# Performance work log

Measured on AMD Instinct MI355X. Metric: run time of the kernel, lower is better.

Reference implementation:

```python
import jax, jax.numpy as jnp
import numpy as np

B, C, T = 16, 768, 1024
STEPS, NNEG, OFFSET = 12, 10, 1
COPIES = NNEG + 1


def setup_inputs() -> dict:
    key = jax.random.key(0)
    k1, k2, k3, k4 = jax.random.split(key, 4)
    x = jax.random.normal(k1, (B, C, T), jnp.float32)
    y = jax.random.normal(k2, (B, C, T), jnp.float32)
    # ConvTranspose2d(in_dim, out_dim, (1, steps)) weight -> [C_in, C_out, steps]
    W = jax.random.normal(k3, (C, C, STEPS), jnp.float32) * 0.02
    b = jnp.zeros((C,), jnp.float32)
    # Negative-sample indices, replicating torch sample_negatives (sample_distance=None):
    # randint in [0, T-1), bump collisions with the positive timestep, add per-batch offset.
    neg = jax.random.randint(k4, (B, NNEG * T), 0, T - 1)
    tszs = jnp.repeat(jnp.arange(T), NNEG)  # [NNEG*T]
    neg = jnp.where(neg >= tszs[None, :], neg + 1, neg)
    neg = neg + jnp.arange(B)[:, None] * T  # index into flattened [B*T]
    return {"x": x, "y": y, "W": W, "b": b, "neg_idxs": neg}


def reference(x, y, W, b, neg_idxs):
    # project_to_steps: ConvTranspose2d with kernel (1, STEPS) on [B,C,T,1] -> [B,C,T,STEPS]
    proj = jnp.einsum('bct,cds->bdts', x, W) + b[None, :, None, None]

    # gather negatives: y -> [C, B*T], fancy-index, reshape to [NNEG, B, C, T]
    yf = jnp.transpose(y, (1, 0, 2)).reshape(C, B * T)
    negs = yf[:, neg_idxs.reshape(-1)].reshape(C, B, NNEG, T)
    negs = jnp.transpose(negs, (2, 1, 0, 3))  # [NNEG, B, C, T]

    targets = jnp.concatenate([y[None], negs], axis=0)  # [COPIES, B, C, T]

    steps = min(STEPS, T - OFFSET)
    preds = []
    for i in range(steps):  # small fixed loop over prediction steps (ragged slice sizes)
        off = i + OFFSET
        # [T-off, B, COPIES]: dot context at step i with targets shifted by off
        p = jnp.einsum('bct,nbct->tbn', proj[..., :T - off, i], targets[..., off:])
        preds.append(p.reshape(-1))
    predictions = jnp.concatenate(preds).reshape(-1, COPIES)  # infonce logits
    labels = jnp.zeros((predictions.shape[0],), jnp.int32)  # positive is copy 0
    return predictions, labels
```

## Files before the change

### kernel.cpp

```cpp
#include <hip/hip_runtime.h>

typedef __bf16 bf16;
typedef __attribute__((ext_vector_type(8))) __bf16 bf16x8;
typedef __attribute__((ext_vector_type(4))) __bf16 bf16x4;
typedef __attribute__((ext_vector_type(4))) float f32x4;

#define B_ 16
#define C_ 768
#define T_ 1024
#define S_ 12
#define NNEG_ 10
#define NCOPY 11
#define NPRED_ROWS 195360
#define NPRED (NPRED_ROWS * NCOPY)

__device__ __forceinline__ void gload16(const void* g, void* l) {
    __builtin_amdgcn_global_load_lds(
        (__attribute__((address_space(1))) void*)g,
        (__attribute__((address_space(3))) void*)l, 16, 0, 0);
}

__global__ void k_wt(const float* __restrict__ W, bf16* __restrict__ WtT) {
    int id = blockIdx.x * blockDim.x + threadIdx.x;
    if (id >= C_ * C_) return;
    int d = id / C_, c = id % C_;
    const float* src = W + ((size_t)c * C_ + d) * S_;
#pragma unroll
    for (int s = 0; s < S_; ++s)
        WtT[(size_t)s * C_ * C_ + id] = (bf16)src[s];
}

__global__ void k_tr2(const float* __restrict__ x, const float* __restrict__ y,
                      bf16* __restrict__ xTc, bf16* __restrict__ yTc, int b0, int cb) {
    __shared__ float tile[32][33];
    int zz = blockIdx.z;
    const float* src = (zz < cb) ? x : y;
    bf16* dst = (zz < cb) ? xTc : yTc;
    int bb = (zz < cb) ? zz : zz - cb;
    int b = b0 + bb;
    int c0 = blockIdx.y * 32, t0 = blockIdx.x * 32;
    int tx = threadIdx.x & 31, ty = threadIdx.x >> 5;
#pragma unroll
    for (int i = 0; i < 4; ++i)
        tile[ty + i * 8][tx] = src[((size_t)b * C_ + c0 + ty + i * 8) * T_ + t0 + tx];
    __syncthreads();
#pragma unroll
    for (int i = 0; i < 4; ++i)
        dst[((size_t)bb * T_ + t0 + ty + i * 8) * C_ + c0 + tx] = (bf16)tile[tx][ty + i * 8];
}

__global__ __launch_bounds__(512, 4) void k_gemm(
    const bf16* __restrict__ xTc, const bf16* __restrict__ WtT,
    const float* __restrict__ bias, bf16* __restrict__ P)
{
    const int nblk = blockIdx.x;
    const int tblk = blockIdx.y;
    const int bb   = blockIdx.z;
    const int tid  = threadIdx.x;
    const int wave = tid >> 6, lane = tid & 63;
    const int mwz = wave >> 2, nwz = wave & 3;
    const int quad = lane >> 4, l15 = lane & 15;

    __shared__ __align__(16) bf16 sA[8][64][8];
    __shared__ __align__(16) bf16 sB[16][64][8];

    const int colk = quad * 8;
    const bf16* gA  = WtT + (size_t)(nblk * 128 + wave * 16 + l15) * C_ + colk;
    const bf16* gB0 = xTc + ((size_t)bb * T_ + tblk * 256 + 2 * wave * 16 + l15) * C_ + colk;
    const bf16* gB1 = gB0 + (size_t)16 * C_;

    f32x4 acc[4][4] = {};

    for (int k0 = 0; k0 < C_; k0 += 32) {
        __syncthreads();
        gload16(gA  + k0, &sA[wave][0][0]);
        gload16(gB0 + k0, &sB[2 * wave][0][0]);
        gload16(gB1 + k0, &sB[2 * wave + 1][0][0]);
        __syncthreads();

        bf16x8 af[4], bfr[4];
#pragma unroll
        for (int i = 0; i < 4; ++i) af[i]  = *(const bf16x8*)&sA[mwz * 4 + i][lane][0];
#pragma unroll
        for (int j = 0; j < 4; ++j) bfr[j] = *(const bf16x8*)&sB[nwz * 4 + j][lane][0];
#pragma unroll
        for (int i = 0; i < 4; ++i)
#pragma unroll
            for (int j = 0; j < 4; ++j)
                acc[i][j] = __builtin_amdgcn_mfma_f32_16x16x32_bf16(af[i], bfr[j], acc[i][j], 0, 0, 0);
    }

#pragma unroll
    for (int i = 0; i < 4; ++i) {
        const int nb = mwz * 64 + i * 16 + quad * 4;
        const f32x4 bv = *(const f32x4*)&bias[(nblk % 6) * 128 + nb];
#pragma unroll
        for (int j = 0; j < 4; ++j) {
            const int t = tblk * 256 + nwz * 64 + j * 16 + l15;
            bf16x4 v;
#pragma unroll
            for (int r = 0; r < 4; ++r) v[r] = (bf16)(acc[i][j][r] + bv[r]);
            *(bf16x4*)&P[((size_t)bb * T_ + t) * (size_t)(S_ * C_) + (size_t)nblk * 128 + nb] = v;
        }
    }
}

__global__ __launch_bounds__(256) void k_pred(
    const bf16* __restrict__ P, const bf16* __restrict__ yTc,
    const int* __restrict__ neg, float* __restrict__ out, int b0)
{
    const int widx = (blockIdx.x << 2) + (threadIdx.x >> 6);
    const int lane = threadIdx.x & 63;
    const int bb = widx >> 10, tp = widx & 1023;
    const int b = b0 + bb;
    const int quad = lane >> 4, l15 = lane & 15;

    int sA = l15 < S_ ? l15 : S_ - 1;
    int tA = tp - 1 - sA;
    if (tA < 0) tA = 0;
    const bf16* arow = P + ((size_t)bb * T_ + tA) * (S_ * C_) + sA * C_ + quad * 8;

    int ridx;
    if (l15 == 0)            ridx = bb * T_ + tp;
    else if (l15 < NCOPY)    ridx = neg[(size_t)b * (NNEG_ * T_) + (l15 - 1) * T_ + tp] - b0 * T_;
    else                     ridx = bb * T_ + tp;
    const bf16* brow = yTc + (size_t)ridx * C_ + quad * 8;

    f32x4 acc = {};
#pragma unroll 4
    for (int kt = 0; kt < C_ / 32; ++kt) {
        bf16x8 av = *(const bf16x8*)(arow + kt * 32);
        bf16x8 bv = *(const bf16x8*)(brow + kt * 32);
        acc = __builtin_amdgcn_mfma_f32_16x16x32_bf16(av, bv, acc, 0, 0, 0);
    }

#pragma unroll
    for (int r = 0; r < 4; ++r) {
        int s = quad * 4 + r;
        int t = tp - 1 - s;
        if (s < S_ && t >= 0) {
            int rowbase = s * (T_ - 1) - (s * (s - 1)) / 2;
            size_t row = (size_t)(rowbase + t) * B_ + b;
            if (l15 < NCOPY)       out[row * NCOPY + l15] = acc[r];
            else if (l15 == NCOPY) out[NPRED + row] = 0.0f;
        }
    }
}

extern "C" void kernel_launch(void* const* d_in, const int* in_sizes, int n_in,
                              void* d_out, int out_size, void* d_ws, size_t ws_size,
                              hipStream_t stream) {
    const float* x    = (const float*)d_in[0];
    const float* y    = (const float*)d_in[1];
    const float* W    = (const float*)d_in[2];
    const float* bias = (const float*)d_in[3];
    const int*   neg  = (const int*)d_in[4];
    float* out = (float*)d_out;

    const size_t offW    = (size_t)S_ * C_ * C_ * 2;
    const size_t perb_xy = (size_t)T_ * C_ * 2;
    const size_t perb_p  = (size_t)T_ * S_ * C_ * 2;
    const size_t perb    = 2 * perb_xy + perb_p;

    int bchunk = (int)((ws_size - offW) / perb);
    if (bchunk < 1) bchunk = 1;
    if (bchunk > B_) bchunk = B_;

    char* ws = (char*)d_ws;
    bf16* WtT = (bf16*)ws;
    bf16* xTc = (bf16*)(ws + offW);
    bf16* yTc = (bf16*)(ws + offW + (size_t)bchunk * perb_xy);
    bf16* P   = (bf16*)(ws + offW + (size_t)bchunk * perb_xy * 2);

    k_wt<<<dim3((C_ * C_ + 255) / 256), 256, 0, stream>>>(W, WtT);

    for (int b0 = 0; b0 < B_;) {
        int cb = bchunk < (B_ - b0) ? bchunk : (B_ - b0);
        k_tr2<<<dim3(T_ / 32, C_ / 32, 2 * cb), 256, 0, stream>>>(x, y, xTc, yTc, b0, cb);
        k_gemm<<<dim3(72, 4, cb), 512, 0, stream>>>(xTc, WtT, bias, P);
        k_pred<<<dim3(cb * 256), 256, 0, stream>>>(P, yTc, neg, out, b0);
        b0 += cb;
    }
}
```

Before: 667.3 us.

## Replace projection GEMM with 256x256 double-buffered swizzled LDS pipelined kernel

Rewrites the projection GEMM to use 256x256 output tiles with K-step 64, double-buffered LDS staging via direct global-to-LDS loads, XOR-swizzled LDS layout, interleaved load/MFMA phases with explicit waitcnt/barriers and setprio, and a remapped 1D grid that spreads blocks across XCDs. The intent is to raise MFMA utilization by overlapping memory and compute and increasing data reuse per block. It uses much more LDS and registers (launch bounds lowered to 2 blocks/CU) and hand-tuned wait counts that must match the issued loads exactly. The grid remap assumes cb*144 is divisible by 8.

Measured after the change: 643.8 us. 1.04x faster.

```diff
diff --git a/kernel.cpp b/kernel.cpp
--- a/kernel.cpp
+++ b/kernel.cpp
@@ -13,6 +13,7 @@
 #define NCOPY 11
 #define NPRED_ROWS 195360
 #define NPRED (NPRED_ROWS * NCOPY)
+#define NT_ 12
 
 __device__ __forceinline__ void gload16(const void* g, void* l) {
     __builtin_amdgcn_global_load_lds(
@@ -49,60 +50,174 @@
         dst[((size_t)bb * T_ + t0 + ty + i * 8) * C_ + c0 + tx] = (bf16)tile[tx][ty + i * 8];
 }
 
-__global__ __launch_bounds__(512, 4) void k_gemm(
+#define SBAR()  __builtin_amdgcn_s_barrier()
+#define SCHED() __builtin_amdgcn_sched_barrier(0)
+#define LGKM0() asm volatile("s_waitcnt lgkmcnt(0)" ::: "memory")
+
+__global__ __launch_bounds__(512, 2) void k_gemm8(
     const bf16* __restrict__ xTc, const bf16* __restrict__ WtT,
     const float* __restrict__ bias, bf16* __restrict__ P)
 {
-    const int nblk = blockIdx.x;
-    const int tblk = blockIdx.y;
-    const int bb   = blockIdx.z;
+    const int q    = gridDim.x >> 3;
+    const int orig = blockIdx.x;
+    const int id2  = (orig & 7) * q + (orig >> 3);
+    const int bb   = id2 / 144;
+    const int rem  = id2 % 144;
+    const int tblk = rem / 36;
+    const int nblk = rem % 36;
+
     const int tid  = threadIdx.x;
-    const int wave = tid >> 6, lane = tid & 63;
-    const int mwz = wave >> 2, nwz = wave & 3;
+    const int wv   = tid >> 6, lane = tid & 63;
+    const int mwz  = wv >> 2, nwz = wv & 3;
     const int quad = lane >> 4, l15 = lane & 15;
 
-    __shared__ __align__(16) bf16 sA[8][64][8];
-    __shared__ __align__(16) bf16 sB[16][64][8];
-
-    const int colk = quad * 8;
-    const bf16* gA  = WtT + (size_t)(nblk * 128 + wave * 16 + l15) * C_ + colk;
-    const bf16* gB0 = xTc + ((size_t)bb * T_ + tblk * 256 + 2 * wave * 16 + l15) * C_ + colk;
-    const bf16* gB1 = gB0 + (size_t)16 * C_;
-
-    f32x4 acc[4][4] = {};
-
-    for (int k0 = 0; k0 < C_; k0 += 32) {
-        __syncthreads();
-        gload16(gA  + k0, &sA[wave][0][0]);
-        gload16(gB0 + k0, &sB[2 * wave][0][0]);
-        gload16(gB1 + k0, &sB[2 * wave + 1][0][0]);
-        __syncthreads();
-
-        bf16x8 af[4], bfr[4];
-#pragma unroll
-        for (int i = 0; i < 4; ++i) af[i]  = *(const bf16x8*)&sA[mwz * 4 + i][lane][0];
-#pragma unroll
-        for (int j = 0; j < 4; ++j) bfr[j] = *(const bf16x8*)&sB[nwz * 4 + j][lane][0];
-#pragma unroll
-        for (int i = 0; i < 4; ++i)
-#pragma unroll
-            for (int j = 0; j < 4; ++j)
-                acc[i][j] = __builtin_amdgcn_mfma_f32_16x16x32_bf16(af[i], bfr[j], acc[i][j], 0, 0, 0);
-    }
-
-#pragma unroll
-    for (int i = 0; i < 4; ++i) {
-        const int nb = mwz * 64 + i * 16 + quad * 4;
-        const f32x4 bv = *(const f32x4*)&bias[(nblk % 6) * 128 + nb];
-#pragma unroll
-        for (int j = 0; j < 4; ++j) {
-            const int t = tblk * 256 + nwz * 64 + j * 16 + l15;
+    __shared__ __align__(16) bf16 sA[2][256][64];
+    __shared__ __align__(16) bf16 sB[2][256][64];
+
+    const int lrow = lane >> 3;
+    const int laneOff = lrow * 1536 + (((lane & 7) * 16) ^ (lrow << 4));
+    const char* aG = (const char*)(WtT + (size_t)(nblk * 256) * C_) + laneOff;
+    const char* bG = (const char*)(xTc + ((size_t)bb * T_ + tblk * 256) * C_) + laneOff;
+    const int h0 = wv * 16, h1 = wv * 16 + 8;
+    const int arw0 = (h0 & 63) + ((h0 >> 6) << 7);
+    const int arw1 = (h1 & 63) + ((h1 >> 6) << 7);
+    const int brw0 = (h0 & 31) + ((h0 >> 5) << 6);
+    const int brw1 = (h1 & 31) + ((h1 >> 5) << 6);
+
+#define STAGE_A(bufn, roff, kt) do { \
+    gload16(aG + (size_t)(arw0 + (roff)) * 1536 + (kt) * 128, &sA[bufn][arw0 + (roff)][0]); \
+    gload16(aG + (size_t)(arw1 + (roff)) * 1536 + (kt) * 128, &sA[bufn][arw1 + (roff)][0]); \
+} while (0)
+#define STAGE_B(bufn, roff, kt) do { \
+    gload16(bG + (size_t)(brw0 + (roff)) * 1536 + (kt) * 128, &sB[bufn][brw0 + (roff)][0]); \
+    gload16(bG + (size_t)(brw1 + (roff)) * 1536 + (kt) * 128, &sB[bufn][brw1 + (roff)][0]); \
+} while (0)
+
+    const int csw0 = (quad * 16) ^ ((l15 & 7) << 4);
+    const int csw1 = (64 + quad * 16) ^ ((l15 & 7) << 4);
+    const char* aRd0 = (const char*)&sA[0][mwz * 128 + l15][0] + csw0;
+    const char* aRd1 = (const char*)&sA[0][mwz * 128 + l15][0] + csw1;
+    const char* bRd0 = (const char*)&sB[0][nwz * 64 + l15][0] + csw0;
+    const char* bRd1 = (const char*)&sB[0][nwz * 64 + l15][0] + csw1;
+
+    f32x4 acc[8][4] = {};
+
+    STAGE_A(0, 0, 0);
+    STAGE_A(0, 64, 0);
+    STAGE_B(0, 32, 0);
+    STAGE_B(0, 0, 0);
+    STAGE_A(1, 0, 1);
+    STAGE_B(1, 32, 1);
+    STAGE_A(1, 64, 1);
+    asm volatile("s_waitcnt vmcnt(6)" ::: "memory");
+    SCHED(); SBAR(); SCHED();
+
+#pragma unroll 2
+    for (int j = 0; j < NT_; ++j) {
+        const int cur = j & 1;
+        const int coff = cur << 15;
+        const char* aC0 = aRd0 + coff; const char* aC1 = aRd1 + coff;
+        const char* bC0 = bRd0 + coff; const char* bC1 = bRd1 + coff;
+
+        bf16x8 a03[4][2], a47[4][2], b01[2][2], b23[2][2], b01p[2][2];
+
+        if (j + 1 < NT_) STAGE_B(cur ^ 1, 0, j + 1);
+#pragma unroll
+        for (int i = 0; i < 4; ++i) {
+            a03[i][0] = *(const bf16x8*)(aC0 + i * 2048);
+            a03[i][1] = *(const bf16x8*)(aC1 + i * 2048);
+        }
+#pragma unroll
+        for (int i = 0; i < 2; ++i) {
+            b01[i][0] = *(const bf16x8*)(bC0 + i * 2048);
+            b01[i][1] = *(const bf16x8*)(bC1 + i * 2048);
+        }
+        SCHED(); SBAR(); LGKM0(); SCHED();
+        __builtin_amdgcn_s_setprio(1);
+#pragma unroll
+        for (int i = 0; i < 4; ++i)
+#pragma unroll
+            for (int n = 0; n < 2; ++n)
+#pragma unroll
+                for (int kk = 0; kk < 2; ++kk)
+                    acc[i][n] = __builtin_amdgcn_mfma_f32_16x16x32_bf16(a03[i][kk], b01[n][kk], acc[i][n], 0, 0, 0);
+        __builtin_amdgcn_s_setprio(0);
+        SCHED(); SBAR(); SCHED();
+
+        if (j + 2 < NT_) STAGE_A(cur, 0, j + 2);
+#pragma unroll
+        for (int i = 0; i < 2; ++i) {
+            b23[i][0] = *(const bf16x8*)(bC0 + 4096 + i * 2048);
+            b23[i][1] = *(const bf16x8*)(bC1 + 4096 + i * 2048);
+        }
+        SCHED(); SBAR(); LGKM0(); SCHED();
+        __builtin_amdgcn_s_setprio(1);
+#pragma unroll
+        for (int i = 0; i < 4; ++i)
+#pragma unroll
+            for (int n = 0; n < 2; ++n)
+#pragma unroll
+                for (int kk = 0; kk < 2; ++kk)
+                    acc[i][2 + n] = __builtin_amdgcn_mfma_f32_16x16x32_bf16(a03[i][kk], b23[n][kk], acc[i][2 + n], 0, 0, 0);
+        __builtin_amdgcn_s_setprio(0);
+        SCHED(); SBAR(); SCHED();
+
+        if (j + 2 < NT_) STAGE_B(cur, 32, j + 2);
+#pragma unroll
+        for (int i = 0; i < 4; ++i) {
+            a47[i][0] = *(const bf16x8*)(aC0 + 8192 + i * 2048);
+            a47[i][1] = *(const bf16x8*)(aC1 + 8192 + i * 2048);
+        }
+        SCHED(); SBAR(); LGKM0(); SCHED();
+        __builtin_amdgcn_s_setprio(1);
+#pragma unroll
+        for (int i = 0; i < 4; ++i)
+#pragma unroll
+            for (int n = 0; n < 2; ++n)
+#pragma unroll
+                for (int kk = 0; kk < 2; ++kk)
+                    acc[4 + i][2 + n] = __builtin_amdgcn_mfma_f32_16x16x32_bf16(a47[i][kk], b23[n][kk], acc[4 + i][2 + n], 0, 0, 0);
+        __builtin_amdgcn_s_setprio(0);
+        SCHED(); SBAR(); SCHED();
+
+        if (j + 2 < NT_) STAGE_A(cur, 64, j + 2);
+#pragma unroll
+        for (int i = 0; i < 2; ++i) {
+            b01p[i][0] = *(const bf16x8*)(bC0 + i * 2048);
+            b01p[i][1] = *(const bf16x8*)(bC1 + i * 2048);
+        }
+        if (j < NT_ - 2)       { asm volatile("s_waitcnt vmcnt(6)" ::: "memory"); }
+        else if (j == NT_ - 2) { asm volatile("s_waitcnt vmcnt(0)" ::: "memory"); }
+        SCHED(); SBAR(); LGKM0(); SCHED();
+        __builtin_amdgcn_s_setprio(1);
+#pragma unroll
+        for (int i = 0; i < 4; ++i)
+#pragma unroll
+            for (int n = 0; n < 2; ++n)
+#pragma unroll
+                for (int kk = 0; kk < 2; ++kk)
+                    acc[4 + i][n] = __builtin_amdgcn_mfma_f32_16x16x32_bf16(a47[i][kk], b01p[n][kk], acc[4 + i][n], 0, 0, 0);
+        __builtin_amdgcn_s_setprio(0);
+        SCHED(); SBAR(); SCHED();
+    }
+
+    const size_t SC = (size_t)S_ * C_;
+    bf16* Pb = P + ((size_t)bb * T_) * SC;
+#pragma unroll
+    for (int i = 0; i < 8; ++i) {
+        const int nloc = mwz * 128 + i * 16 + quad * 4;
+        const f32x4 bv = *(const f32x4*)&bias[(nblk % 3) * 256 + nloc];
+#pragma unroll
+        for (int n = 0; n < 4; ++n) {
+            const int t = tblk * 256 + nwz * 64 + n * 16 + l15;
             bf16x4 v;
 #pragma unroll
-            for (int r = 0; r < 4; ++r) v[r] = (bf16)(acc[i][j][r] + bv[r]);
-            *(bf16x4*)&P[((size_t)bb * T_ + t) * (size_t)(S_ * C_) + (size_t)nblk * 128 + nb] = v;
-        }
-    }
+            for (int r = 0; r < 4; ++r) v[r] = (bf16)(acc[i][n][r] + bv[r]);
+            *(bf16x4*)&Pb[(size_t)t * SC + nblk * 256 + nloc] = v;
+        }
+    }
+#undef STAGE_A
+#undef STAGE_B
 }
 
 __global__ __launch_bounds__(256) void k_pred(
@@ -177,7 +292,7 @@
     for (int b0 = 0; b0 < B_;) {
         int cb = bchunk < (B_ - b0) ? bchunk : (B_ - b0);
         k_tr2<<<dim3(T_ / 32, C_ / 32, 2 * cb), 256, 0, stream>>>(x, y, xTc, yTc, b0, cb);
-        k_gemm<<<dim3(72, 4, cb), 512, 0, stream>>>(xTc, WtT, bias, P);
+        k_gemm8<<<dim3(cb * 144), 512, 0, stream>>>(xTc, WtT, bias, P);
         k_pred<<<dim3(cb * 256), 256, 0, stream>>>(P, yTc, neg, out, b0);
         b0 += cb;
     }
```
